# Kernel tuning notes

Hardware: AMD Instinct MI355X
Metric: run time of the kernel (lower is better)

Reference implementation:

```python
import jax, jax.numpy as jnp
import numpy as np

# Bit-slice quantization config (MSB-first; first 1-bit slice is the sign slice)
INPUT_SLICE = (1, 2, 2, 2)    # 7 bits total
WEIGHT_SLICE = (1, 2, 2, 2)   # 7 bits total
INPUT_GRAN = 32               # input quant granularity along K (per unfolded row)
WEIGHT_GRAN_K = 32            # weight quant granularity along K
WEIGHT_GRAN_N = 32            # weight quant granularity along N
STRIDE = 1
PAD = 1
KSIZE = 3


def _quantize(x, max_abs, total_bits):
    """Symmetric per-granule quantization to signed total_bits integers."""
    max_val = float((1 << (total_bits - 1)) - 1)
    scale = max_abs / max_val
    scale = jnp.where(scale == 0, jnp.ones_like(scale), scale)
    q = jnp.clip(jnp.round(x / scale), -max_val, max_val)
    return q, scale


def _slice_recombine(q, slice_bits):
    """Emulate the bit-slice path: decompose signed int q (two's complement)
    into slices per slice_bits (MSB first), then recombine exactly as the
    crossbar MapReduce accumulation 'sum_i slice_i * 2^offset_i' would."""
    t = int(sum(slice_bits))
    qi = q.astype(jnp.int32)
    u = jnp.where(qi < 0, qi + (1 << t), qi)  # two's complement unsigned rep
    recomb = jnp.zeros_like(u)
    off = t
    for b in slice_bits:  # fixed, small slice loop
        off -= b
        s = (u >> off) & ((1 << b) - 1)
        recomb = recomb + (s << off)
    recomb = jnp.where(recomb >= (1 << (t - 1)), recomb - (1 << t), recomb)
    return recomb.astype(jnp.float32)


def _fake_quant_input(x):
    # x: (B, L, K) unfolded activations; granularity (1, INPUT_GRAN)
    B, L, K = x.shape
    g = INPUT_GRAN
    xg = x.reshape(B, L, K // g, g)
    max_abs = jnp.max(jnp.abs(xg), axis=-1, keepdims=True)
    q, scale = _quantize(xg, max_abs, sum(INPUT_SLICE))
    q = _slice_recombine(q, INPUT_SLICE)
    deq = (q * scale).reshape(B, L, K)
    # straight-through estimator (matches custom autograd conv2d_mem_func)
    return x + jax.lax.stop_gradient(deq - x)


def _fake_quant_weight(w):
    # w: (K, N) reshaped weight; granularity (WEIGHT_GRAN_K, WEIGHT_GRAN_N)
    K, N = w.shape
    gk, gn = WEIGHT_GRAN_K, WEIGHT_GRAN_N
    wg = w.reshape(K // gk, gk, N // gn, gn)
    max_abs = jnp.max(jnp.abs(wg), axis=(1, 3), keepdims=True)
    q, scale = _quantize(wg, max_abs, sum(WEIGHT_SLICE))
    q = _slice_recombine(q, WEIGHT_SLICE)
    deq = (q * scale).reshape(K, N)
    return w + jax.lax.stop_gradient(deq - w)


def _unfold(x, k, stride, pad):
    # torch.F.unfold semantics -> (B, L, C*k*k), C-major ordering
    B, C, H, W = x.shape
    xp = jnp.pad(x, ((0, 0), (0, 0), (pad, pad), (pad, pad)))
    Ho = (H + 2 * pad - k) // stride + 1
    Wo = (W + 2 * pad - k) // stride + 1
    cols = []
    for ki in range(k):  # fixed small kernel loop
        for kj in range(k):
            cols.append(xp[:, :, ki:ki + stride * Ho:stride, kj:kj + stride * Wo:stride])
    patches = jnp.stack(cols, axis=2)              # (B, C, k*k, Ho, Wo)
    patches = patches.reshape(B, C * k * k, Ho * Wo)
    return patches.transpose(0, 2, 1), Ho, Wo      # (B, L, K)


def setup_inputs() -> dict:
    key = jax.random.key(0)
    k1, k2, k3 = jax.random.split(key, 3)
    B, C, H, W = 8, 256, 56, 56
    N = 256
    fan_in = C * KSIZE * KSIZE
    x = jax.random.normal(k1, (B, C, H, W), dtype=jnp.float32)
    weight = jax.random.normal(k2, (N, C, KSIZE, KSIZE), dtype=jnp.float32) / np.sqrt(fan_in)
    bias = jax.random.normal(k3, (N,), dtype=jnp.float32) / np.sqrt(fan_in)
    return {"input": x, "weight": weight, "bias": bias}


def reference(input, weight, bias):
    B = input.shape[0]
    N = weight.shape[0]
    cols, Ho, Wo = _unfold(input, KSIZE, STRIDE, PAD)     # (B, L, K)
    w2d = weight.reshape(N, -1).T                         # (K, N)
    xq = _fake_quant_input(cols)
    wq = _fake_quant_weight(w2d)
    out = jnp.einsum('blk,kn->bln', xq, wq) + bias        # (B, L, N)
    out = out.transpose(0, 2, 1).reshape(B, N, Ho, Wo)    # fold with 1x1 kernel
    return out
```

## Files before the change

kernel.cpp:

```cpp
#include <hip/hip_runtime.h>
#include <hip/hip_bf16.h>
#include <stdint.h>

#define KD 2304
#define LD 3136
#define ND 256
#define MD 25088
#define CD 256
#define PITCH 64
#define PROWS 58
#define PLANE (PROWS * PITCH)

typedef __bf16 bf16x8 __attribute__((ext_vector_type(8)));
typedef float f32x4 __attribute__((ext_vector_type(4)));
typedef float f32x4u __attribute__((ext_vector_type(4), aligned(4)));

__device__ __forceinline__ void gload_lds16(const void* g, void* l) {
  __builtin_amdgcn_global_load_lds(
      (const __attribute__((address_space(1))) unsigned int*)g,
      (__attribute__((address_space(3))) unsigned int*)l, 16, 0, 0);
}

__global__ __launch_bounds__(256) void pad_kernel(
    const float* __restrict__ x, float* __restrict__ xpad) {
  const int plane = blockIdx.x;
  const float* src = x + (size_t)plane * LD;
  float* dst = xpad + (size_t)plane * PLANE;
  const int cc4 = (threadIdx.x & 15) * 4;
  const int r0 = threadIdx.x >> 4;
#pragma unroll
  for (int p = 0; p < 4; ++p) {
    const int r = r0 + p * 16;
    if (r >= PROWS) continue;
    f32x4 o = {0.f, 0.f, 0.f, 0.f};
    if (r >= 1 && r <= 56) {
      const float* srow = src + (r - 1) * 56;
      if (cc4 == 0) {
        f32x4u v = *(const f32x4u*)(srow);
        o[1] = v[0]; o[2] = v[1]; o[3] = v[2];
      } else if (cc4 <= 52) {
        o = *(const f32x4u*)(srow + cc4 - 1);
      } else if (cc4 == 56) {
        f32x4u v = *(const f32x4u*)(srow + 52);
        o[0] = v[3];
      }
    }
    *(f32x4*)(dst + r * PITCH + cc4) = o;
  }
}

__global__ __launch_bounds__(256) void quant_w_kernel(
    const float* __restrict__ w, __hip_bfloat16* __restrict__ wqT) {
  const int gk = blockIdx.x % 72;
  const int gn = blockIdx.x / 72;
  const int n = gn * 32 + (threadIdx.x >> 3);
  const int k = gk * 32 + (threadIdx.x & 7) * 4;
  const float4 v = *(const float4*)(w + (size_t)n * KD + k);
  float a = fmaxf(fmaxf(fabsf(v.x), fabsf(v.y)), fmaxf(fabsf(v.z), fabsf(v.w)));
#pragma unroll
  for (int m = 1; m <= 32; m <<= 1) a = fmaxf(a, __shfl_xor(a, m, 64));
  __shared__ float red[4];
  if ((threadIdx.x & 63) == 0) red[threadIdx.x >> 6] = a;
  __syncthreads();
  const float mx = fmaxf(fmaxf(red[0], red[1]), fmaxf(red[2], red[3]));
  const float r63 = (mx == 0.f) ? 0.f : 63.f / mx;
  const float scale = mx * (1.f / 63.f);
  ushort4 o;
  o.x = __builtin_bit_cast(unsigned short, __float2bfloat16(rintf(v.x * r63) * scale));
  o.y = __builtin_bit_cast(unsigned short, __float2bfloat16(rintf(v.y * r63) * scale));
  o.z = __builtin_bit_cast(unsigned short, __float2bfloat16(rintf(v.z * r63) * scale));
  o.w = __builtin_bit_cast(unsigned short, __float2bfloat16(rintf(v.w * r63) * scale));
  *(ushort4*)((unsigned short*)wqT + (size_t)n * KD + k) = o;
}

__device__ __forceinline__ void qload_u(const float* __restrict__ pb, int p0,
                                        int c0, f32x4u (&win)[5][3]) {
#pragma unroll
  for (int dc = 0; dc < 5; ++dc) {
    const int cdc = (c0 + dc > 255) ? 255 : c0 + dc;
    const float* cp = pb + p0 + cdc * PLANE;
#pragma unroll
    for (int di = 0; di < 3; ++di)
      win[dc][di] = *(const f32x4u*)(cp + di * PITCH);
  }
}

template <int KP0>
__device__ __forceinline__ void qfinish(const f32x4u (&win)[5][3],
                                        char* as_row, unsigned cbase, unsigned swz) {
  float v[32];
#pragma unroll
  for (int t = 0; t < 32; ++t) {
    const int idx = KP0 + t;
    v[t] = win[idx / 9][(idx % 9) / 3][(idx % 9) % 3];
  }
  float m16[16];
#pragma unroll
  for (int t = 0; t < 16; ++t)
    m16[t] = fmaxf(__builtin_fabsf(v[2 * t]), __builtin_fabsf(v[2 * t + 1]));
#pragma unroll
  for (int t = 0; t < 8; ++t) m16[t] = fmaxf(m16[t], m16[t + 8]);
#pragma unroll
  for (int t = 0; t < 4; ++t) m16[t] = fmaxf(m16[t], m16[t + 4]);
  const float mx = fmaxf(fmaxf(m16[0], m16[1]), fmaxf(m16[2], m16[3]));
  float r63 = 63.f * __builtin_amdgcn_rcpf(mx);
  r63 = (mx == 0.f) ? 0.f : r63;
  const float scale = mx * (1.f / 63.f);
  unsigned pk[16];
#pragma unroll
  for (int t = 0; t < 16; ++t) {
    const float a = rintf(v[2 * t] * r63) * scale;
    const float b = rintf(v[2 * t + 1] * r63) * scale;
    unsigned d;
    asm("v_cvt_pk_bf16_f32 %0, %1, %2" : "=v"(d) : "v"(a), "v"(b));
    pk[t] = d;
  }
#pragma unroll
  for (int s = 0; s < 4; ++s) {
    uint4 o = {pk[4 * s], pk[4 * s + 1], pk[4 * s + 2], pk[4 * s + 3]};
    *(uint4*)(as_row + ((cbase + (unsigned)(s * 16)) ^ swz)) = o;
  }
}

__device__ __forceinline__ void stage_ns(const unsigned short* __restrict__ wsrc,
                                         int k0, int lane, int w, char* Ns) {
#pragma unroll
  for (int sg = 0; sg < 16; ++sg) {
    const int c = w * 16 + sg;
    const int rowN = c * 4 + (lane >> 4);
    const int u = (lane & 15) ^ (rowN & 7);
    gload_lds16(wsrc + (size_t)rowN * KD + k0 + u * 8,
                Ns + c * 1024 + lane * 16);
  }
}

__device__ __forceinline__ void mfma_phase(const char* As, const char* Ns,
                                           f32x4 (&acc)[4][4], int w, int lq, int hv) {
  const unsigned swq = (unsigned)((lq & 7) << 4);
#pragma unroll
  for (int kk = 0; kk < 4; ++kk) {
    const unsigned ko = (unsigned)(kk * 64 + hv * 16);
    bf16x8 af[4], bfr[4];
#pragma unroll
    for (int ifr = 0; ifr < 4; ++ifr) {
      const unsigned rn = (unsigned)(w * 64 + ifr * 16 + lq);
      af[ifr] = *(const bf16x8*)(Ns + rn * 256u + (ko ^ swq));
    }
#pragma unroll
    for (int jfr = 0; jfr < 4; ++jfr) {
      const unsigned rm = (unsigned)(jfr * 16 + lq);
      bfr[jfr] = *(const bf16x8*)(As + rm * 256u + (ko ^ swq));
    }
#pragma unroll
    for (int ifr = 0; ifr < 4; ++ifr)
#pragma unroll
      for (int jfr = 0; jfr < 4; ++jfr)
        acc[ifr][jfr] = __builtin_amdgcn_mfma_f32_16x16x32_bf16(
            af[ifr], bfr[jfr], acc[ifr][jfr], 0, 0, 0);
  }
}

__global__ __launch_bounds__(256, 2) void fused_gemm_kernel(
    const float* __restrict__ xpad, const __hip_bfloat16* __restrict__ wqT,
    const float* __restrict__ bias, float* __restrict__ out) {
  extern __shared__ char smem[];
  char* As = smem;
  char* Ns = smem + 16384;
  const int tid = threadIdx.x;
  const int lane = tid & 63;
  const int w = __builtin_amdgcn_readfirstlane(tid >> 6);

  const int bid = blockIdx.x;
  const int mt = (bid & 7) * 49 + (bid >> 3);
  const int m0 = mt * 64;

  const int b = m0 / LD;
  const int l = m0 - b * LD + lane;
  const int i = l / 56;
  const int j = l - i * 56;
  const float* pb = xpad + (size_t)b * CD * PLANE;
  const int p0 = i * PITCH + j;
  char* as_row = As + lane * 256;
  const unsigned swz = (unsigned)((lane & 7) << 4);
  const unsigned cbase = (unsigned)(w * 64);
  const unsigned short* wqTu = (const unsigned short*)wqT;

  const int lq = lane & 15, hv = lane >> 4;

  f32x4 acc[4][4] = {};
  f32x4u win[5][3];

  int kbase = 32 * w;
  int ph = (32 * w) % 9;
  qload_u(pb, p0, kbase / 9, win);

  for (int R = 0; R < 18; ++R) {
    stage_ns(wqTu, R * 128, lane, w, Ns);

    switch (ph) {
      case 0: qfinish<0>(win, as_row, cbase, swz); break;
      case 1: qfinish<1>(win, as_row, cbase, swz); break;
      case 2: qfinish<2>(win, as_row, cbase, swz); break;
      case 3: qfinish<3>(win, as_row, cbase, swz); break;
      case 4: qfinish<4>(win, as_row, cbase, swz); break;
      case 5: qfinish<5>(win, as_row, cbase, swz); break;
      case 6: qfinish<6>(win, as_row, cbase, swz); break;
      default: qfinish<7>(win, as_row, cbase, swz); break;
      case 8: qfinish<8>(win, as_row, cbase, swz); break;
    }

    kbase += 128;
    ph += 2; if (ph >= 9) ph -= 9;
    qload_u(pb, p0, kbase / 9, win);

    asm volatile("s_waitcnt vmcnt(15) lgkmcnt(0)\n\ts_barrier" ::: "memory");
    __builtin_amdgcn_sched_barrier(0);

    mfma_phase(As, Ns, acc, w, lq, hv);

    asm volatile("s_waitcnt lgkmcnt(0)\n\ts_barrier" ::: "memory");
    __builtin_amdgcn_sched_barrier(0);
  }

#pragma unroll
  for (int ifr = 0; ifr < 4; ++ifr) {
    const int nb = w * 64 + ifr * 16 + hv * 4;
    const float4 b4 = *(const float4*)&bias[nb];
#pragma unroll
    for (int jfr = 0; jfr < 4; ++jfr) {
      const int m = m0 + jfr * 16 + lq;
      const int ll = m - b * LD;
      float* op = out + ((size_t)b * ND + nb) * LD + ll;
      op[0]      = acc[ifr][jfr].x + b4.x;
      op[LD]     = acc[ifr][jfr].y + b4.y;
      op[2 * LD] = acc[ifr][jfr].z + b4.z;
      op[3 * LD] = acc[ifr][jfr].w + b4.w;
    }
  }
}

extern "C" void kernel_launch(void* const* d_in, const int* in_sizes, int n_in,
                              void* d_out, int out_size, void* d_ws, size_t ws_size,
                              hipStream_t stream) {
  const float* x = (const float*)d_in[0];
  const float* wgt = (const float*)d_in[1];
  const float* bias = (const float*)d_in[2];
  float* out = (float*)d_out;

  float* xpad = (float*)d_ws;
  __hip_bfloat16* wqT = (__hip_bfloat16*)((char*)d_ws + 30408704);

  pad_kernel<<<8 * CD, 256, 0, stream>>>(x, xpad);
  quant_w_kernel<<<576, 256, 0, stream>>>(wgt, wqT);
  fused_gemm_kernel<<<392, 256, 80 * 1024, stream>>>(xpad, wqT, bias, out);
}
```

Measured before the change: 77.66 us.

## Split GEMM N dimension into two 128-wide tiles to double grid size

The fused GEMM block now computes a 64x128 output tile instead of 64x256, doubling the grid to 784 blocks with a 2x2 wave layout, static shared memory of 48KB and an occupancy hint of 3. The weight staging and LDS swizzle are adjusted to a 16-way XOR pattern. The aim is better CU fill and latency hiding on 256 CUs. The trade-off is that each M tile's input quantization and im2col staging is now done twice, once per N half, which adds redundant global loads and ALU work.

```diff
diff --git a/kernel.cpp b/kernel.cpp
--- a/kernel.cpp
+++ b/kernel.cpp
@@ -124,55 +124,60 @@
 
 __device__ __forceinline__ void stage_ns(const unsigned short* __restrict__ wsrc,
                                          int k0, int lane, int w, char* Ns) {
-#pragma unroll
-  for (int sg = 0; sg < 16; ++sg) {
-    const int c = w * 16 + sg;
-    const int rowN = c * 4 + (lane >> 4);
-    const int u = (lane & 15) ^ (rowN & 7);
+  const int hv4 = lane >> 4;
+#pragma unroll
+  for (int sg = 0; sg < 8; ++sg) {
+    const int c = w * 8 + sg;
+    const int rowN = c * 4 + hv4;
+    const int u = (lane & 15) ^ (rowN & 15);
     gload_lds16(wsrc + (size_t)rowN * KD + k0 + u * 8,
                 Ns + c * 1024 + lane * 16);
   }
 }
 
 __device__ __forceinline__ void mfma_phase(const char* As, const char* Ns,
-                                           f32x4 (&acc)[4][4], int w, int lq, int hv) {
-  const unsigned swq = (unsigned)((lq & 7) << 4);
+                                           f32x4 (&acc)[4][2], int wn, int wm,
+                                           int lq, int hv) {
+  const unsigned swq = (unsigned)(lq << 4);
 #pragma unroll
   for (int kk = 0; kk < 4; ++kk) {
     const unsigned ko = (unsigned)(kk * 64 + hv * 16);
-    bf16x8 af[4], bfr[4];
+    bf16x8 af[4], bfr[2];
 #pragma unroll
     for (int ifr = 0; ifr < 4; ++ifr) {
-      const unsigned rn = (unsigned)(w * 64 + ifr * 16 + lq);
+      const unsigned rn = (unsigned)(wn * 64 + ifr * 16 + lq);
       af[ifr] = *(const bf16x8*)(Ns + rn * 256u + (ko ^ swq));
     }
 #pragma unroll
-    for (int jfr = 0; jfr < 4; ++jfr) {
-      const unsigned rm = (unsigned)(jfr * 16 + lq);
+    for (int jfr = 0; jfr < 2; ++jfr) {
+      const unsigned rm = (unsigned)(wm * 32 + jfr * 16 + lq);
       bfr[jfr] = *(const bf16x8*)(As + rm * 256u + (ko ^ swq));
     }
 #pragma unroll
     for (int ifr = 0; ifr < 4; ++ifr)
 #pragma unroll
-      for (int jfr = 0; jfr < 4; ++jfr)
+      for (int jfr = 0; jfr < 2; ++jfr)
         acc[ifr][jfr] = __builtin_amdgcn_mfma_f32_16x16x32_bf16(
             af[ifr], bfr[jfr], acc[ifr][jfr], 0, 0, 0);
   }
 }
 
-__global__ __launch_bounds__(256, 2) void fused_gemm_kernel(
+__global__ __launch_bounds__(256, 3) void fused_gemm_kernel(
     const float* __restrict__ xpad, const __hip_bfloat16* __restrict__ wqT,
     const float* __restrict__ bias, float* __restrict__ out) {
-  extern __shared__ char smem[];
-  char* As = smem;
-  char* Ns = smem + 16384;
+  __shared__ char As[64 * 256];
+  __shared__ char Ns[128 * 256];
   const int tid = threadIdx.x;
   const int lane = tid & 63;
   const int w = __builtin_amdgcn_readfirstlane(tid >> 6);
 
   const int bid = blockIdx.x;
-  const int mt = (bid & 7) * 49 + (bid >> 3);
+  const int xcd = bid & 7;
+  const int idx = bid >> 3;
+  const int mt = xcd * 49 + (idx >> 1);
+  const int nt = idx & 1;
   const int m0 = mt * 64;
+  const int n1 = nt * 128;
 
   const int b = m0 / LD;
   const int l = m0 - b * LD + lane;
@@ -181,13 +186,14 @@
   const float* pb = xpad + (size_t)b * CD * PLANE;
   const int p0 = i * PITCH + j;
   char* as_row = As + lane * 256;
-  const unsigned swz = (unsigned)((lane & 7) << 4);
+  const unsigned swz = (unsigned)((lane & 15) << 4);
   const unsigned cbase = (unsigned)(w * 64);
-  const unsigned short* wqTu = (const unsigned short*)wqT;
+  const unsigned short* wsrc = (const unsigned short*)wqT + (size_t)n1 * KD;
 
   const int lq = lane & 15, hv = lane >> 4;
-
-  f32x4 acc[4][4] = {};
+  const int wn = w & 1, wm = w >> 1;
+
+  f32x4 acc[4][2] = {};
   f32x4u win[5][3];
 
   int kbase = 32 * w;
@@ -195,7 +201,7 @@
   qload_u(pb, p0, kbase / 9, win);
 
   for (int R = 0; R < 18; ++R) {
-    stage_ns(wqTu, R * 128, lane, w, Ns);
+    stage_ns(wsrc, R * 128, lane, w, Ns);
 
     switch (ph) {
       case 0: qfinish<0>(win, as_row, cbase, swz); break;
@@ -216,7 +222,7 @@
     asm volatile("s_waitcnt vmcnt(15) lgkmcnt(0)\n\ts_barrier" ::: "memory");
     __builtin_amdgcn_sched_barrier(0);
 
-    mfma_phase(As, Ns, acc, w, lq, hv);
+    mfma_phase(As, Ns, acc, wn, wm, lq, hv);
 
     asm volatile("s_waitcnt lgkmcnt(0)\n\ts_barrier" ::: "memory");
     __builtin_amdgcn_sched_barrier(0);
@@ -224,11 +230,11 @@
 
 #pragma unroll
   for (int ifr = 0; ifr < 4; ++ifr) {
-    const int nb = w * 64 + ifr * 16 + hv * 4;
+    const int nb = n1 + wn * 64 + ifr * 16 + hv * 4;
     const float4 b4 = *(const float4*)&bias[nb];
 #pragma unroll
-    for (int jfr = 0; jfr < 4; ++jfr) {
-      const int m = m0 + jfr * 16 + lq;
+    for (int jfr = 0; jfr < 2; ++jfr) {
+      const int m = m0 + wm * 32 + jfr * 16 + lq;
       const int ll = m - b * LD;
       float* op = out + ((size_t)b * ND + nb) * LD + ll;
       op[0]      = acc[ifr][jfr].x + b4.x;
@@ -252,5 +258,5 @@
 
   pad_kernel<<<8 * CD, 256, 0, stream>>>(x, xpad);
   quant_w_kernel<<<576, 256, 0, stream>>>(wgt, wqT);
-  fused_gemm_kernel<<<392, 256, 80 * 1024, stream>>>(xpad, wqT, bias, out);
-}
+  fused_gemm_kernel<<<784, 256, 0, stream>>>(xpad, wqT, bias, out);
+}
```

New measurement: 97.70 us. +25.8%, slower.

## Restructure fused GEMM to 8 waves with triple-buffered A and staggered quantization

Applied to the files above, without the earlier changes.

The fused conv GEMM moves from 4 waves per block with a 128-wide K step to 8 waves with a 64-wide K step. Waves are split 4 along N and 2 along M, and the quantized A tile is triple-buffered in LDS. Each group of two waves quantizes one future A tile every fourth iteration, so the quantization work is spread out and overlapped with the MFMA phases of other waves. Input window loads are specialized per phase to skip unused rows, and MFMA sections get raised priority via setprio. The cost is twice as many barriers per K step and a full vmcnt(0) wait each iteration, which could stall behind the global loads.

```diff
diff --git a/kernel.cpp b/kernel.cpp
--- a/kernel.cpp
+++ b/kernel.cpp
@@ -73,21 +73,29 @@
   *(ushort4*)((unsigned short*)wqT + (size_t)n * KD + k) = o;
 }
 
-__device__ __forceinline__ void qload_u(const float* __restrict__ pb, int p0,
-                                        int c0, f32x4u (&win)[5][3]) {
+template <int KP0>
+__device__ __forceinline__ void qloadT(const float* __restrict__ pb, int p0, int c0,
+                                       f32x4u (&win)[5][3]) {
+  constexpr int NCH = (KP0 + 31) / 9 + 1;
 #pragma unroll
   for (int dc = 0; dc < 5; ++dc) {
+    if (dc >= NCH) continue;
+    const int tlo = (dc == 0) ? KP0 : 0;
+    const int thi = (dc == NCH - 1) ? (KP0 + 31 - 9 * (NCH - 1)) : 8;
     const int cdc = (c0 + dc > 255) ? 255 : c0 + dc;
     const float* cp = pb + p0 + cdc * PLANE;
 #pragma unroll
-    for (int di = 0; di < 3; ++di)
-      win[dc][di] = *(const f32x4u*)(cp + di * PITCH);
+    for (int di = 0; di < 3; ++di) {
+      if (di >= tlo / 3 && di <= thi / 3)
+        win[dc][di] = *(const f32x4u*)(cp + di * PITCH);
+    }
   }
 }
 
 template <int KP0>
-__device__ __forceinline__ void qfinish(const f32x4u (&win)[5][3],
-                                        char* as_row, unsigned cbase, unsigned swz) {
+__device__ __forceinline__ void qfinishT(const f32x4u (&win)[5][3],
+                                         char* __restrict__ as_base,
+                                         int lane, unsigned cbase) {
   float v[32];
 #pragma unroll
   for (int t = 0; t < 32; ++t) {
@@ -115,57 +123,87 @@
     asm("v_cvt_pk_bf16_f32 %0, %1, %2" : "=v"(d) : "v"(a), "v"(b));
     pk[t] = d;
   }
+  char* row = as_base + lane * 128;
+  const unsigned swz = (unsigned)((lane & 7) << 4);
 #pragma unroll
   for (int s = 0; s < 4; ++s) {
     uint4 o = {pk[4 * s], pk[4 * s + 1], pk[4 * s + 2], pk[4 * s + 3]};
-    *(uint4*)(as_row + ((cbase + (unsigned)(s * 16)) ^ swz)) = o;
-  }
-}
+    *(uint4*)(row + ((cbase + (unsigned)(s * 16)) ^ swz)) = o;
+  }
+}
+
+#define SW_FIN(PH, DST, CB)                                                   \
+  switch (PH) {                                                               \
+    case 0: qfinishT<0>(win, DST, lane, CB); break;                           \
+    case 1: qfinishT<1>(win, DST, lane, CB); break;                           \
+    case 2: qfinishT<2>(win, DST, lane, CB); break;                           \
+    case 3: qfinishT<3>(win, DST, lane, CB); break;                           \
+    case 4: qfinishT<4>(win, DST, lane, CB); break;                           \
+    case 5: qfinishT<5>(win, DST, lane, CB); break;                           \
+    case 6: qfinishT<6>(win, DST, lane, CB); break;                           \
+    case 7: qfinishT<7>(win, DST, lane, CB); break;                           \
+    default: qfinishT<8>(win, DST, lane, CB); break;                          \
+  }
+
+#define SW_LOAD(PH, C0)                                                       \
+  switch (PH) {                                                               \
+    case 0: qloadT<0>(pb, p0, C0, win); break;                                \
+    case 1: qloadT<1>(pb, p0, C0, win); break;                                \
+    case 2: qloadT<2>(pb, p0, C0, win); break;                                \
+    case 3: qloadT<3>(pb, p0, C0, win); break;                                \
+    case 4: qloadT<4>(pb, p0, C0, win); break;                                \
+    case 5: qloadT<5>(pb, p0, C0, win); break;                                \
+    case 6: qloadT<6>(pb, p0, C0, win); break;                                \
+    case 7: qloadT<7>(pb, p0, C0, win); break;                                \
+    default: qloadT<8>(pb, p0, C0, win); break;                               \
+  }
 
 __device__ __forceinline__ void stage_ns(const unsigned short* __restrict__ wsrc,
-                                         int k0, int lane, int w, char* Ns) {
-#pragma unroll
-  for (int sg = 0; sg < 16; ++sg) {
-    const int c = w * 16 + sg;
-    const int rowN = c * 4 + (lane >> 4);
-    const int u = (lane & 15) ^ (rowN & 7);
-    gload_lds16(wsrc + (size_t)rowN * KD + k0 + u * 8,
-                Ns + c * 1024 + lane * 16);
-  }
-}
-
-__device__ __forceinline__ void mfma_phase(const char* As, const char* Ns,
-                                           f32x4 (&acc)[4][4], int w, int lq, int hv) {
-  const unsigned swq = (unsigned)((lq & 7) << 4);
-#pragma unroll
-  for (int kk = 0; kk < 4; ++kk) {
-    const unsigned ko = (unsigned)(kk * 64 + hv * 16);
-    bf16x8 af[4], bfr[4];
-#pragma unroll
-    for (int ifr = 0; ifr < 4; ++ifr) {
-      const unsigned rn = (unsigned)(w * 64 + ifr * 16 + lq);
-      af[ifr] = *(const bf16x8*)(Ns + rn * 256u + (ko ^ swq));
-    }
-#pragma unroll
-    for (int jfr = 0; jfr < 4; ++jfr) {
-      const unsigned rm = (unsigned)(jfr * 16 + lq);
-      bfr[jfr] = *(const bf16x8*)(As + rm * 256u + (ko ^ swq));
-    }
-#pragma unroll
-    for (int ifr = 0; ifr < 4; ++ifr)
-#pragma unroll
-      for (int jfr = 0; jfr < 4; ++jfr)
-        acc[ifr][jfr] = __builtin_amdgcn_mfma_f32_16x16x32_bf16(
-            af[ifr], bfr[jfr], acc[ifr][jfr], 0, 0, 0);
-  }
-}
-
-__global__ __launch_bounds__(256, 2) void fused_gemm_kernel(
+                                         int k0, int lane, int w,
+                                         char* __restrict__ Ns) {
+#pragma unroll
+  for (int sg = 0; sg < 4; ++sg) {
+    const int c = w * 4 + sg;
+    const int row = c * 8 + (lane >> 3);
+    const int u = (lane & 7) ^ (row & 7);
+    gload_lds16(wsrc + (size_t)row * KD + k0 + u * 8, Ns + c * 1024 + lane * 16);
+  }
+}
+
+__device__ __forceinline__ void mfma_phase(const char* __restrict__ AsC,
+                                           const char* __restrict__ Ns,
+                                           f32x4 (&acc)[4][2], int w, int lq, int hv) {
+  const int wn = w & 3, wm = w >> 2;
+#pragma unroll
+  for (int kk = 0; kk < 2; ++kk) {
+    bf16x8 af[4], bf[2];
+#pragma unroll
+    for (int i = 0; i < 4; ++i) {
+      const unsigned rn = (unsigned)(wn * 64 + i * 16 + lq);
+      const unsigned u = (unsigned)((kk * 4 + hv) ^ (rn & 7));
+      af[i] = *(const bf16x8*)(Ns + rn * 128u + u * 16u);
+    }
+#pragma unroll
+    for (int j = 0; j < 2; ++j) {
+      const unsigned rm = (unsigned)(wm * 32 + j * 16 + lq);
+      const unsigned u = (unsigned)((kk * 4 + hv) ^ (rm & 7));
+      bf[j] = *(const bf16x8*)(AsC + rm * 128u + u * 16u);
+    }
+#pragma unroll
+    for (int i = 0; i < 4; ++i)
+#pragma unroll
+      for (int j = 0; j < 2; ++j)
+        acc[i][j] = __builtin_amdgcn_mfma_f32_16x16x32_bf16(
+            af[i], bf[j], acc[i][j], 0, 0, 0);
+  }
+}
+
+__global__ __launch_bounds__(512, 4) void fused_gemm_kernel(
     const float* __restrict__ xpad, const __hip_bfloat16* __restrict__ wqT,
     const float* __restrict__ bias, float* __restrict__ out) {
-  extern __shared__ char smem[];
+  __shared__ char smem[56 * 1024];
   char* As = smem;
-  char* Ns = smem + 16384;
+  char* Ns = smem + 24576;
   const int tid = threadIdx.x;
   const int lane = tid & 63;
   const int w = __builtin_amdgcn_readfirstlane(tid >> 6);
@@ -180,61 +218,72 @@
   const int j = l - i * 56;
   const float* pb = xpad + (size_t)b * CD * PLANE;
   const int p0 = i * PITCH + j;
-  char* as_row = As + lane * 256;
-  const unsigned swz = (unsigned)((lane & 7) << 4);
-  const unsigned cbase = (unsigned)(w * 64);
-  const unsigned short* wqTu = (const unsigned short*)wqT;
-
+  const unsigned short* wsrc = (const unsigned short*)wqT;
+
+  const int slot = w & 1;
+  const int g = w >> 1;
+  const unsigned cb = (unsigned)(slot * 64);
   const int lq = lane & 15, hv = lane >> 4;
 
-  f32x4 acc[4][4] = {};
+  f32x4 acc[4][2] = {};
   f32x4u win[5][3];
 
-  int kbase = 32 * w;
-  int ph = (32 * w) % 9;
-  qload_u(pb, p0, kbase / 9, win);
-
-  for (int R = 0; R < 18; ++R) {
-    stage_ns(wqTu, R * 128, lane, w, Ns);
-
-    switch (ph) {
-      case 0: qfinish<0>(win, as_row, cbase, swz); break;
-      case 1: qfinish<1>(win, as_row, cbase, swz); break;
-      case 2: qfinish<2>(win, as_row, cbase, swz); break;
-      case 3: qfinish<3>(win, as_row, cbase, swz); break;
-      case 4: qfinish<4>(win, as_row, cbase, swz); break;
-      case 5: qfinish<5>(win, as_row, cbase, swz); break;
-      case 6: qfinish<6>(win, as_row, cbase, swz); break;
-      default: qfinish<7>(win, as_row, cbase, swz); break;
-      case 8: qfinish<8>(win, as_row, cbase, swz); break;
-    }
-
-    kbase += 128;
-    ph += 2; if (ph >= 9) ph -= 9;
-    qload_u(pb, p0, kbase / 9, win);
-
-    asm volatile("s_waitcnt vmcnt(15) lgkmcnt(0)\n\ts_barrier" ::: "memory");
+  if (g < 2) {
+    const int kp = 64 * g + 32 * slot;
+    const int php = kp % 9;
+    SW_LOAD(php, kp / 9);
+    char* dst = As + g * 8192;
+    SW_FIN(php, dst, cb);
+  }
+  int kq = 64 * (g + 2) + 32 * slot;
+  int phq = kq % 9;
+  {
+    const int c0 = kq / 9;
+    SW_LOAD(phq, c0);
+  }
+  asm volatile("s_waitcnt lgkmcnt(0)\n\ts_barrier" ::: "memory");
+  __builtin_amdgcn_sched_barrier(0);
+
+  for (int R = 0; R < 36; ++R) {
+    stage_ns(wsrc, R * 64, lane, w, Ns);
+
+    const bool qi = ((R & 3) == g);
+    if (qi && R + 2 <= 35) {
+      char* dst = As + ((R + 2) % 3) * 8192;
+      SW_FIN(phq, dst, cb);
+    }
+
+    asm volatile("s_waitcnt vmcnt(0) lgkmcnt(0)\n\ts_barrier" ::: "memory");
     __builtin_amdgcn_sched_barrier(0);
 
-    mfma_phase(As, Ns, acc, w, lq, hv);
+    __builtin_amdgcn_s_setprio(1);
+    mfma_phase(As + (R % 3) * 8192, Ns, acc, w, lq, hv);
+    __builtin_amdgcn_s_setprio(0);
+
+    if (qi && R + 6 <= 35) {
+      kq += 256;
+      phq += 4; if (phq >= 9) phq -= 9;
+      const int c0 = kq / 9;
+      SW_LOAD(phq, c0);
+    }
 
     asm volatile("s_waitcnt lgkmcnt(0)\n\ts_barrier" ::: "memory");
     __builtin_amdgcn_sched_barrier(0);
   }
 
 #pragma unroll
-  for (int ifr = 0; ifr < 4; ++ifr) {
-    const int nb = w * 64 + ifr * 16 + hv * 4;
+  for (int i4 = 0; i4 < 4; ++i4) {
+    const int nb = (w & 3) * 64 + i4 * 16 + hv * 4;
     const float4 b4 = *(const float4*)&bias[nb];
 #pragma unroll
-    for (int jfr = 0; jfr < 4; ++jfr) {
-      const int m = m0 + jfr * 16 + lq;
+    for (int j2 = 0; j2 < 2; ++j2) {
+      const int m = m0 + (w >> 2) * 32 + j2 * 16 + lq;
       const int ll = m - b * LD;
       float* op = out + ((size_t)b * ND + nb) * LD + ll;
-      op[0]      = acc[ifr][jfr].x + b4.x;
-      op[LD]     = acc[ifr][jfr].y + b4.y;
-      op[2 * LD] = acc[ifr][jfr].z + b4.z;
-      op[3 * LD] = acc[ifr][jfr].w + b4.w;
+      op[0]      = acc[i4][j2].x + b4.x;
+      op[LD]     = acc[i4][j2].y + b4.y;
+      op[2 * LD] = acc[i4][j2].z + b4.z;
+      op[3 * LD] = acc[i4][j2].w + b4.w;
     }
   }
 }
@@ -252,5 +301,5 @@
 
   pad_kernel<<<8 * CD, 256, 0, stream>>>(x, xpad);
   quant_w_kernel<<<576, 256, 0, stream>>>(wgt, wqT);
-  fused_gemm_kernel<<<392, 256, 80 * 1024, stream>>>(xpad, wqT, bias, out);
-}
+  fused_gemm_kernel<<<392, 512, 0, stream>>>(xpad, wqT, bias, out);
+}
```

After: 105.4 us. 35.7% more time.

## Merge prep kernels and split LDS tiles into two 64-wide K halves

Applied to the files above, without the earlier changes.

Merges the padding and weight-quantization kernels into one launch, removing a kernel launch and the gap between the two. Splits the A and N shared-memory tiles into two 64-element K halves, each with 128-byte rows and its own XOR swizzle, and stages the weight tile with 8 rows of 8 chunks per instruction. Raises wave priority around the MFMA phase. The new layout changes LDS bank access patterns and how the staging loads are shaped, and the combined launch may schedule blocks differently.

```diff
diff --git a/kernel.cpp b/kernel.cpp
--- a/kernel.cpp
+++ b/kernel.cpp
@@ -21,56 +21,57 @@
       (__attribute__((address_space(3))) unsigned int*)l, 16, 0, 0);
 }
 
-__global__ __launch_bounds__(256) void pad_kernel(
-    const float* __restrict__ x, float* __restrict__ xpad) {
-  const int plane = blockIdx.x;
-  const float* src = x + (size_t)plane * LD;
-  float* dst = xpad + (size_t)plane * PLANE;
-  const int cc4 = (threadIdx.x & 15) * 4;
-  const int r0 = threadIdx.x >> 4;
-#pragma unroll
-  for (int p = 0; p < 4; ++p) {
-    const int r = r0 + p * 16;
-    if (r >= PROWS) continue;
-    f32x4 o = {0.f, 0.f, 0.f, 0.f};
-    if (r >= 1 && r <= 56) {
-      const float* srow = src + (r - 1) * 56;
-      if (cc4 == 0) {
-        f32x4u v = *(const f32x4u*)(srow);
-        o[1] = v[0]; o[2] = v[1]; o[3] = v[2];
-      } else if (cc4 <= 52) {
-        o = *(const f32x4u*)(srow + cc4 - 1);
-      } else if (cc4 == 56) {
-        f32x4u v = *(const f32x4u*)(srow + 52);
-        o[0] = v[3];
+__global__ __launch_bounds__(256) void prep_kernel(
+    const float* __restrict__ x, float* __restrict__ xpad,
+    const float* __restrict__ w, __hip_bfloat16* __restrict__ wqT) {
+  if (blockIdx.x < 2048) {
+    const int plane = blockIdx.x;
+    const float* src = x + (size_t)plane * LD;
+    float* dst = xpad + (size_t)plane * PLANE;
+    const int cc4 = (threadIdx.x & 15) * 4;
+    const int r0 = threadIdx.x >> 4;
+#pragma unroll
+    for (int p = 0; p < 4; ++p) {
+      const int r = r0 + p * 16;
+      if (r >= PROWS) continue;
+      f32x4 o = {0.f, 0.f, 0.f, 0.f};
+      if (r >= 1 && r <= 56) {
+        const float* srow = src + (r - 1) * 56;
+        if (cc4 == 0) {
+          f32x4u v = *(const f32x4u*)(srow);
+          o[1] = v[0]; o[2] = v[1]; o[3] = v[2];
+        } else if (cc4 <= 52) {
+          o = *(const f32x4u*)(srow + cc4 - 1);
+        } else if (cc4 == 56) {
+          f32x4u v = *(const f32x4u*)(srow + 52);
+          o[0] = v[3];
+        }
       }
-    }
-    *(f32x4*)(dst + r * PITCH + cc4) = o;
-  }
-}
-
-__global__ __launch_bounds__(256) void quant_w_kernel(
-    const float* __restrict__ w, __hip_bfloat16* __restrict__ wqT) {
-  const int gk = blockIdx.x % 72;
-  const int gn = blockIdx.x / 72;
-  const int n = gn * 32 + (threadIdx.x >> 3);
-  const int k = gk * 32 + (threadIdx.x & 7) * 4;
-  const float4 v = *(const float4*)(w + (size_t)n * KD + k);
-  float a = fmaxf(fmaxf(fabsf(v.x), fabsf(v.y)), fmaxf(fabsf(v.z), fabsf(v.w)));
-#pragma unroll
-  for (int m = 1; m <= 32; m <<= 1) a = fmaxf(a, __shfl_xor(a, m, 64));
-  __shared__ float red[4];
-  if ((threadIdx.x & 63) == 0) red[threadIdx.x >> 6] = a;
-  __syncthreads();
-  const float mx = fmaxf(fmaxf(red[0], red[1]), fmaxf(red[2], red[3]));
-  const float r63 = (mx == 0.f) ? 0.f : 63.f / mx;
-  const float scale = mx * (1.f / 63.f);
-  ushort4 o;
-  o.x = __builtin_bit_cast(unsigned short, __float2bfloat16(rintf(v.x * r63) * scale));
-  o.y = __builtin_bit_cast(unsigned short, __float2bfloat16(rintf(v.y * r63) * scale));
-  o.z = __builtin_bit_cast(unsigned short, __float2bfloat16(rintf(v.z * r63) * scale));
-  o.w = __builtin_bit_cast(unsigned short, __float2bfloat16(rintf(v.w * r63) * scale));
-  *(ushort4*)((unsigned short*)wqT + (size_t)n * KD + k) = o;
+      *(f32x4*)(dst + r * PITCH + cc4) = o;
+    }
+  } else {
+    const int wb = blockIdx.x - 2048;
+    const int gk = wb % 72;
+    const int gn = wb / 72;
+    const int n = gn * 32 + (threadIdx.x >> 3);
+    const int k = gk * 32 + (threadIdx.x & 7) * 4;
+    const float4 v = *(const float4*)(w + (size_t)n * KD + k);
+    float a = fmaxf(fmaxf(fabsf(v.x), fabsf(v.y)), fmaxf(fabsf(v.z), fabsf(v.w)));
+#pragma unroll
+    for (int m = 1; m <= 32; m <<= 1) a = fmaxf(a, __shfl_xor(a, m, 64));
+    __shared__ float red[4];
+    if ((threadIdx.x & 63) == 0) red[threadIdx.x >> 6] = a;
+    __syncthreads();
+    const float mx = fmaxf(fmaxf(red[0], red[1]), fmaxf(red[2], red[3]));
+    const float r63 = (mx == 0.f) ? 0.f : 63.f / mx;
+    const float scale = mx * (1.f / 63.f);
+    ushort4 o;
+    o.x = __builtin_bit_cast(unsigned short, __float2bfloat16(rintf(v.x * r63) * scale));
+    o.y = __builtin_bit_cast(unsigned short, __float2bfloat16(rintf(v.y * r63) * scale));
+    o.z = __builtin_bit_cast(unsigned short, __float2bfloat16(rintf(v.z * r63) * scale));
+    o.w = __builtin_bit_cast(unsigned short, __float2bfloat16(rintf(v.w * r63) * scale));
+    *(ushort4*)((unsigned short*)wqT + (size_t)n * KD + k) = o;
+  }
 }
 
 __device__ __forceinline__ void qload_u(const float* __restrict__ pb, int p0,
@@ -86,8 +87,9 @@
 }
 
 template <int KP0>
-__device__ __forceinline__ void qfinish(const f32x4u (&win)[5][3],
-                                        char* as_row, unsigned cbase, unsigned swz) {
+__device__ __forceinline__ void qfinishT(const f32x4u (&win)[5][3],
+                                         char* __restrict__ as_base,
+                                         int lane, unsigned cbase) {
   float v[32];
 #pragma unroll
   for (int t = 0; t < 32; ++t) {
@@ -115,48 +117,68 @@
     asm("v_cvt_pk_bf16_f32 %0, %1, %2" : "=v"(d) : "v"(a), "v"(b));
     pk[t] = d;
   }
+  char* row = as_base + lane * 128;
+  const unsigned swz = (unsigned)((lane & 7) << 4);
 #pragma unroll
   for (int s = 0; s < 4; ++s) {
     uint4 o = {pk[4 * s], pk[4 * s + 1], pk[4 * s + 2], pk[4 * s + 3]};
-    *(uint4*)(as_row + ((cbase + (unsigned)(s * 16)) ^ swz)) = o;
-  }
-}
+    *(uint4*)(row + ((cbase + (unsigned)(s * 16)) ^ swz)) = o;
+  }
+}
+
+#define SW_FIN(PH, DST, CB)                                                   \
+  switch (PH) {                                                               \
+    case 0: qfinishT<0>(win, DST, lane, CB); break;                           \
+    case 1: qfinishT<1>(win, DST, lane, CB); break;                           \
+    case 2: qfinishT<2>(win, DST, lane, CB); break;                           \
+    case 3: qfinishT<3>(win, DST, lane, CB); break;                           \
+    case 4: qfinishT<4>(win, DST, lane, CB); break;                           \
+    case 5: qfinishT<5>(win, DST, lane, CB); break;                           \
+    case 6: qfinishT<6>(win, DST, lane, CB); break;                           \
+    case 7: qfinishT<7>(win, DST, lane, CB); break;                           \
+    default: qfinishT<8>(win, DST, lane, CB); break;                          \
+  }
 
 __device__ __forceinline__ void stage_ns(const unsigned short* __restrict__ wsrc,
-                                         int k0, int lane, int w, char* Ns) {
-#pragma unroll
-  for (int sg = 0; sg < 16; ++sg) {
-    const int c = w * 16 + sg;
-    const int rowN = c * 4 + (lane >> 4);
-    const int u = (lane & 15) ^ (rowN & 7);
-    gload_lds16(wsrc + (size_t)rowN * KD + k0 + u * 8,
-                Ns + c * 1024 + lane * 16);
-  }
-}
-
-__device__ __forceinline__ void mfma_phase(const char* As, const char* Ns,
-                                           f32x4 (&acc)[4][4], int w, int lq, int hv) {
-  const unsigned swq = (unsigned)((lq & 7) << 4);
+                                         int k0, int lane, int w,
+                                         char* __restrict__ NsH) {
+#pragma unroll
+  for (int sg = 0; sg < 8; ++sg) {
+    const int c = w * 8 + sg;
+    const int row = c * 8 + (lane >> 3);
+    const int u = (lane & 7) ^ (row & 7);
+    gload_lds16(wsrc + (size_t)row * KD + k0 + u * 8, NsH + c * 1024 + lane * 16);
+  }
+}
+
+__device__ __forceinline__ void mfma_phase(
+    const char* __restrict__ As0, const char* __restrict__ As1,
+    const char* __restrict__ Ns0, const char* __restrict__ Ns1,
+    f32x4 (&acc)[4][4], int w, int lq, int hv) {
 #pragma unroll
   for (int kk = 0; kk < 4; ++kk) {
-    const unsigned ko = (unsigned)(kk * 64 + hv * 16);
-    bf16x8 af[4], bfr[4];
-#pragma unroll
-    for (int ifr = 0; ifr < 4; ++ifr) {
-      const unsigned rn = (unsigned)(w * 64 + ifr * 16 + lq);
-      af[ifr] = *(const bf16x8*)(Ns + rn * 256u + (ko ^ swq));
-    }
-#pragma unroll
-    for (int jfr = 0; jfr < 4; ++jfr) {
-      const unsigned rm = (unsigned)(jfr * 16 + lq);
-      bfr[jfr] = *(const bf16x8*)(As + rm * 256u + (ko ^ swq));
-    }
-#pragma unroll
-    for (int ifr = 0; ifr < 4; ++ifr)
-#pragma unroll
-      for (int jfr = 0; jfr < 4; ++jfr)
-        acc[ifr][jfr] = __builtin_amdgcn_mfma_f32_16x16x32_bf16(
-            af[ifr], bfr[jfr], acc[ifr][jfr], 0, 0, 0);
+    const char* NsH = (kk < 2) ? Ns0 : Ns1;
+    const char* AsH = (kk < 2) ? As0 : As1;
+    const int kl = kk & 1;
+    bf16x8 af[4], bf[4];
+#pragma unroll
+    for (int i = 0; i < 4; ++i) {
+      const unsigned rn = (unsigned)(w * 64 + i * 16 + lq);
+      const unsigned u = (unsigned)((kl * 4 + hv) ^ (rn & 7));
+      af[i] = *(const bf16x8*)(NsH + rn * 128u + u * 16u);
+    }
+#pragma unroll
+    for (int j = 0; j < 4; ++j) {
+      const unsigned rm = (unsigned)(j * 16 + lq);
+      const unsigned u = (unsigned)((kl * 4 + hv) ^ (rm & 7));
+      bf[j] = *(const bf16x8*)(AsH + rm * 128u + u * 16u);
+    }
+#pragma unroll
+    for (int i = 0; i < 4; ++i)
+#pragma unroll
+      for (int j = 0; j < 4; ++j)
+        acc[i][j] = __builtin_amdgcn_mfma_f32_16x16x32_bf16(
+            af[i], bf[j], acc[i][j], 0, 0, 0);
   }
 }
 
@@ -164,8 +186,10 @@
     const float* __restrict__ xpad, const __hip_bfloat16* __restrict__ wqT,
     const float* __restrict__ bias, float* __restrict__ out) {
   extern __shared__ char smem[];
-  char* As = smem;
-  char* Ns = smem + 16384;
+  char* As0 = smem;
+  char* As1 = smem + 8192;
+  char* Ns0 = smem + 16384;
+  char* Ns1 = smem + 49152;
   const int tid = threadIdx.x;
   const int lane = tid & 63;
   const int w = __builtin_amdgcn_readfirstlane(tid >> 6);
@@ -180,61 +204,54 @@
   const int j = l - i * 56;
   const float* pb = xpad + (size_t)b * CD * PLANE;
   const int p0 = i * PITCH + j;
-  char* as_row = As + lane * 256;
-  const unsigned swz = (unsigned)((lane & 7) << 4);
-  const unsigned cbase = (unsigned)(w * 64);
-  const unsigned short* wqTu = (const unsigned short*)wqT;
-
+  const unsigned short* wsrc = (const unsigned short*)wqT;
+
+  char* as_dst = (w < 2) ? As0 : As1;
+  const unsigned cb = (unsigned)((w & 1) * 64);
   const int lq = lane & 15, hv = lane >> 4;
 
   f32x4 acc[4][4] = {};
   f32x4u win[5][3];
 
-  int kbase = 32 * w;
-  int ph = (32 * w) % 9;
-  qload_u(pb, p0, kbase / 9, win);
+  int kq = 32 * w;
+  int ph = kq % 9;
+  qload_u(pb, p0, kq / 9, win);
 
   for (int R = 0; R < 18; ++R) {
-    stage_ns(wqTu, R * 128, lane, w, Ns);
-
-    switch (ph) {
-      case 0: qfinish<0>(win, as_row, cbase, swz); break;
-      case 1: qfinish<1>(win, as_row, cbase, swz); break;
-      case 2: qfinish<2>(win, as_row, cbase, swz); break;
-      case 3: qfinish<3>(win, as_row, cbase, swz); break;
-      case 4: qfinish<4>(win, as_row, cbase, swz); break;
-      case 5: qfinish<5>(win, as_row, cbase, swz); break;
-      case 6: qfinish<6>(win, as_row, cbase, swz); break;
-      default: qfinish<7>(win, as_row, cbase, swz); break;
-      case 8: qfinish<8>(win, as_row, cbase, swz); break;
-    }
-
-    kbase += 128;
+    stage_ns(wsrc, R * 128, lane, w, Ns0);
+    stage_ns(wsrc, R * 128 + 64, lane, w, Ns1);
+    __builtin_amdgcn_sched_barrier(0);
+
+    SW_FIN(ph, as_dst, cb);
+
+    kq += 128;
     ph += 2; if (ph >= 9) ph -= 9;
-    qload_u(pb, p0, kbase / 9, win);
+    qload_u(pb, p0, kq / 9, win);
 
     asm volatile("s_waitcnt vmcnt(15) lgkmcnt(0)\n\ts_barrier" ::: "memory");
     __builtin_amdgcn_sched_barrier(0);
 
-    mfma_phase(As, Ns, acc, w, lq, hv);
+    __builtin_amdgcn_s_setprio(1);
+    mfma_phase(As0, As1, Ns0, Ns1, acc, w, lq, hv);
+    __builtin_amdgcn_s_setprio(0);
 
     asm volatile("s_waitcnt lgkmcnt(0)\n\ts_barrier" ::: "memory");
     __builtin_amdgcn_sched_barrier(0);
   }
 
 #pragma unroll
-  for (int ifr = 0; ifr < 4; ++ifr) {
-    const int nb = w * 64 + ifr * 16 + hv * 4;
+  for (int i4 = 0; i4 < 4; ++i4) {
+    const int nb = w * 64 + i4 * 16 + hv * 4;
     const float4 b4 = *(const float4*)&bias[nb];
 #pragma unroll
-    for (int jfr = 0; jfr < 4; ++jfr) {
-      const int m = m0 + jfr * 16 + lq;
+    for (int j4 = 0; j4 < 4; ++j4) {
+      const int m = m0 + j4 * 16 + lq;
       const int ll = m - b * LD;
       float* op = out + ((size_t)b * ND + nb) * LD + ll;
-      op[0]      = acc[ifr][jfr].x + b4.x;
-      op[LD]     = acc[ifr][jfr].y + b4.y;
-      op[2 * LD] = acc[ifr][jfr].z + b4.z;
-      op[3 * LD] = acc[ifr][jfr].w + b4.w;
+      op[0]      = acc[i4][j4].x + b4.x;
+      op[LD]     = acc[i4][j4].y + b4.y;
+      op[2 * LD] = acc[i4][j4].z + b4.z;
+      op[3 * LD] = acc[i4][j4].w + b4.w;
     }
   }
 }
@@ -250,7 +267,6 @@
   float* xpad = (float*)d_ws;
   __hip_bfloat16* wqT = (__hip_bfloat16*)((char*)d_ws + 30408704);
 
-  pad_kernel<<<8 * CD, 256, 0, stream>>>(x, xpad);
-  quant_w_kernel<<<576, 256, 0, stream>>>(wgt, wqT);
+  prep_kernel<<<2048 + 576, 256, 0, stream>>>(x, xpad, wgt, wqT);
   fused_gemm_kernel<<<392, 256, 80 * 1024, stream>>>(xpad, wqT, bias, out);
 }
```

New measurement: 70.27 us. 9.5% less time.
